# Performance work log

Hardware: AMD Instinct MI355X
Metric: run time of the kernel (lower is better)

Reference implementation:

```python
import jax, jax.numpy as jnp
import numpy as np

NUM_HEADS = 12


def setup_inputs() -> dict:
    key = jax.random.key(0)
    k1, k2, k3 = jax.random.split(key, 3)
    B, S, D = 2, 2048, 768
    x = jax.random.normal(k1, (B, S, D), dtype=jnp.float32)
    # torch Linear init: normal(std=0.002) weights, zero bias; stored as [in, out]
    W_qkv = jax.random.normal(k2, (D, 3 * D), dtype=jnp.float32) * 0.002
    b_qkv = jnp.zeros((3 * D,), dtype=jnp.float32)
    W_vw = jax.random.normal(k3, (D, D), dtype=jnp.float32) * 0.002
    b_vw = jnp.zeros((D,), dtype=jnp.float32)
    mask = jnp.ones((B, S), dtype=jnp.int32)  # padding mask, all valid
    return {"x": x, "W_qkv": W_qkv, "b_qkv": b_qkv, "W_vw": W_vw, "b_vw": b_vw, "mask": mask}


def reference(x, W_qkv, b_qkv, W_vw, b_vw, mask):
    B, S, D = x.shape
    H = NUM_HEADS
    Dh = D // H
    qkv = (x @ W_qkv + b_qkv).reshape(B, S, 3, H, Dh)
    q, k, v = qkv[:, :, 0], qkv[:, :, 1], qkv[:, :, 2]
    # [B, H, S, S] attention scores (full matrix, as in original)
    w = jnp.einsum('bshd,bzhd->bhsz', q, k)
    w = w / jnp.sqrt(jnp.asarray(Dh, dtype=x.dtype))  # scale=True
    # log-mask trick: padding mask [B,1,1,S] * causal tril [1,1,S,S]
    causal = jnp.tril(jnp.ones((S, S), dtype=x.dtype))
    wholemask = mask.astype(x.dtype)[:, None, None, :] * causal[None, None]
    w = w + jnp.log(wholemask)
    w = jax.nn.softmax(w, axis=-1)
    vw = jnp.einsum('bhsz,bzhd->bshd', w, v).reshape(B, S, D)
    return vw @ W_vw + b_vw
```

## Files before the change

kernel.cpp:

```cpp
#include <hip/hip_runtime.h>
#include <hip/hip_bf16.h>
#include <cmath>
#include <cstddef>

#define B_    2
#define S_    2048
#define D_    768
#define H_    12
#define DH_   64
#define NQKV_ 2304

typedef __attribute__((ext_vector_type(8))) short  short8;
typedef __attribute__((ext_vector_type(4))) float  floatx4;

__device__ __forceinline__ unsigned short f2bf(float f) {
    union { __hip_bfloat16 h; unsigned short u; } cv;
    cv.h = __float2bfloat16(f);
    return cv.u;
}

__device__ __forceinline__ void stage16(const unsigned short* g, unsigned short* ldsbase, int lane) {
#if __has_builtin(__builtin_amdgcn_global_load_lds)
    __builtin_amdgcn_global_load_lds(
        (const __attribute__((address_space(1))) unsigned int*)g,
        (__attribute__((address_space(3))) unsigned int*)ldsbase, 16, 0, 0);
#else
    *(short8*)(ldsbase + lane * 8) = *(const short8*)g;
#endif
}

__global__ void cvt_x_kernel(const float* __restrict__ x, unsigned short* __restrict__ xb)
{
    int i = (blockIdx.x * 256 + threadIdx.x) * 8;
    float4 a = *(const float4*)(x + i);
    float4 b = *(const float4*)(x + i + 4);
    short8 v;
    v[0] = (short)f2bf(a.x); v[1] = (short)f2bf(a.y);
    v[2] = (short)f2bf(a.z); v[3] = (short)f2bf(a.w);
    v[4] = (short)f2bf(b.x); v[5] = (short)f2bf(b.y);
    v[6] = (short)f2bf(b.z); v[7] = (short)f2bf(b.w);
    *(short8*)(xb + i) = v;
}

__global__ void cvt_w_kernel(const float* __restrict__ Wq, const float* __restrict__ Wv,
                             unsigned short* __restrict__ WqT, unsigned short* __restrict__ WvT)
{
    const int z = blockIdx.z;
    const int N = z ? D_ : NQKV_;
    if ((int)blockIdx.x * 32 >= N) return;
    const float* W = z ? Wv : Wq;
    unsigned short* WT = z ? WvT : WqT;

    __shared__ float t[32][33];
    const int tx = threadIdx.x, ty = threadIdx.y;
    const int n0 = blockIdx.x * 32, k0 = blockIdx.y * 32;
    #pragma unroll
    for (int i = 0; i < 4; ++i)
        t[ty + i * 8][tx] = W[(size_t)(k0 + ty + i * 8) * N + n0 + tx];
    __syncthreads();
    #pragma unroll
    for (int i = 0; i < 4; ++i)
        WT[(size_t)(n0 + ty + i * 8) * 768 + k0 + tx] = f2bf(t[tx][ty + i * 8]);
}

__global__ void vt_kernel(const unsigned short* __restrict__ V, unsigned short* __restrict__ VT)
{
    __shared__ unsigned short t[64][72];
    const int bh = blockIdx.x, s0 = blockIdx.y * 64;
    const unsigned short* src = V + ((size_t)bh * S_ + s0) * DH_;
    const int r = threadIdx.x >> 3, c = (threadIdx.x & 7) * 8;
    #pragma unroll
    for (int it = 0; it < 2; ++it)
        *(short8*)&t[r + it * 32][c] = *(const short8*)(src + (size_t)(r + it * 32) * DH_ + c);
    __syncthreads();
    #pragma unroll
    for (int it = 0; it < 2; ++it) {
        int d = r + it * 32;
        short8 v;
        #pragma unroll
        for (int i = 0; i < 8; ++i) v[i] = (short)t[c + i][d];
        *(short8*)(VT + ((size_t)bh * DH_ + d) * S_ + s0 + c) = v;
    }
}

__global__ __launch_bounds__(256, 2)
void mm_qkv_kernel(const unsigned short* __restrict__ A, const unsigned short* __restrict__ BT,
                   const float* __restrict__ bias,
                   unsigned short* __restrict__ Qo, unsigned short* __restrict__ Ko,
                   unsigned short* __restrict__ Vo)
{
    __shared__ unsigned short As[128][32];
    __shared__ unsigned short Bs[128][32];
    const int tid = threadIdx.x;
    const int wid = tid >> 6, lane = tid & 63;
    const int q = lane >> 4, ln = lane & 15;
    const int wm = (wid & 1) * 64, wn = (wid >> 1) * 64;
    const int m0 = blockIdx.y * 128, n0 = blockIdx.x * 128;
    const int lrow = wid * 16 + (lane >> 2);
    const int lcol = (lane & 3) * 8;
    const unsigned short* Ag = A  + (size_t)(m0 + lrow) * 768 + lcol;
    const unsigned short* Bg = BT + (size_t)(n0 + lrow) * 768 + lcol;

    floatx4 acc[4][4] = {};
    for (int k0 = 0; k0 < 768; k0 += 32) {
        __syncthreads();
        stage16(Ag + k0,            &As[wid * 16][0],      lane);
        stage16(Ag + k0 + 64 * 768, &As[64 + wid * 16][0], lane);
        stage16(Bg + k0,            &Bs[wid * 16][0],      lane);
        stage16(Bg + k0 + 64 * 768, &Bs[64 + wid * 16][0], lane);
        __syncthreads();
        short8 af[4], bf[4];
        #pragma unroll
        for (int mt = 0; mt < 4; ++mt) af[mt] = *(const short8*)&As[wm + mt * 16 + ln][q * 8];
        #pragma unroll
        for (int nt = 0; nt < 4; ++nt) bf[nt] = *(const short8*)&Bs[wn + nt * 16 + ln][q * 8];
        #pragma unroll
        for (int mt = 0; mt < 4; ++mt)
            #pragma unroll
            for (int nt = 0; nt < 4; ++nt)
                acc[mt][nt] = __builtin_amdgcn_mfma_f32_16x16x32_bf16(af[mt], bf[nt], acc[mt][nt], 0, 0, 0);
    }

    const int t = n0 / 768;
    unsigned short* __restrict__ dst = (t == 0) ? Qo : ((t == 1) ? Ko : Vo);
    const float qscale = (t == 0) ? 0.18033688011112042f : 1.0f;
    const int colb = n0 - t * 768 + wn;
    float bv[4];
    #pragma unroll
    for (int nt = 0; nt < 4; ++nt) bv[nt] = bias[n0 + wn + nt * 16 + ln];
    #pragma unroll
    for (int mt = 0; mt < 4; ++mt)
        #pragma unroll
        for (int r = 0; r < 4; ++r) {
            int row = m0 + wm + mt * 16 + q * 4 + r;
            int bb = row >> 11, s = row & 2047;
            #pragma unroll
            for (int nt = 0; nt < 4; ++nt) {
                int col = colb + nt * 16 + ln;
                int h = col >> 6, d = col & 63;
                dst[((size_t)(bb * H_ + h) * S_ + s) * DH_ + d] = f2bf((acc[mt][nt][r] + bv[nt]) * qscale);
            }
        }
}

__global__ __launch_bounds__(256, 2)
void flash8_kernel(const unsigned short* __restrict__ Qg, const unsigned short* __restrict__ Kg,
                   const unsigned short* __restrict__ VTg, const int* __restrict__ mask,
                   unsigned short* __restrict__ VW)
{
    __shared__ unsigned short Pl[4][32][40];
    __shared__ float Ol[32][68];
    __shared__ float li_s[4][32];

    const int tid = threadIdx.x;
    const int wid = tid >> 6, lane = tid & 63;
    const int q = lane >> 4, ln = lane & 15;
    const int bh = blockIdx.x % 24;
    const int pix = blockIdx.x / 24;
    const int b = bh / H_, h = bh % H_;

    const unsigned short* Qb = Qg  + (size_t)bh * S_ * DH_;
    const unsigned short* Kb = Kg  + (size_t)bh * S_ * DH_;
    const unsigned short* Vt = VTg + (size_t)bh * DH_ * S_;
    const int* mb = mask + b * S_;

    for (int half = 0; half < 2; ++half) {
        const int qt = half ? (63 - pix) : pix;
        const int r0 = qt * 32;
        const int T = qt + 1;

        short8 qf[2][2];
        #pragma unroll
        for (int mt = 0; mt < 2; ++mt)
            #pragma unroll
            for (int kk = 0; kk < 2; ++kk)
                qf[mt][kk] = *(const short8*)(Qb + (size_t)(r0 + mt * 16 + ln) * DH_ + kk * 32 + q * 8);

        floatx4 o[2][4] = {};
        float li[2][4] = {};

        for (int t = wid; t < T; t += 4) {
            const int z0 = t * 32;

            short8 kb[2][2];
            #pragma unroll
            for (int nt = 0; nt < 2; ++nt)
                #pragma unroll
                for (int kk = 0; kk < 2; ++kk)
                    kb[nt][kk] = *(const short8*)(Kb + (size_t)(z0 + nt * 16 + ln) * DH_ + kk * 32 + q * 8);

            short8 vb[4];
            #pragma unroll
            for (int dt = 0; dt < 4; ++dt)
                vb[dt] = *(const short8*)(Vt + (size_t)(dt * 16 + ln) * S_ + z0 + q * 8);

            const int m0i = mb[z0 + ln];
            const int m1i = mb[z0 + 16 + ln];

            floatx4 s[2][2] = {};
            __builtin_amdgcn_s_setprio(1);
            #pragma unroll
            for (int mt = 0; mt < 2; ++mt)
                #pragma unroll
                for (int nt = 0; nt < 2; ++nt) {
                    s[mt][nt] = __builtin_amdgcn_mfma_f32_16x16x32_bf16(qf[mt][0], kb[nt][0], s[mt][nt], 0, 0, 0);
                    s[mt][nt] = __builtin_amdgcn_mfma_f32_16x16x32_bf16(qf[mt][1], kb[nt][1], s[mt][nt], 0, 0, 0);
                }
            __builtin_amdgcn_s_setprio(0);

            const bool diag = (z0 + 31 > r0);
            if (__all(m0i && m1i) && !diag) {
                #pragma unroll
                for (int mt = 0; mt < 2; ++mt)
                    #pragma unroll
                    for (int nt = 0; nt < 2; ++nt)
                        #pragma unroll
                        for (int r = 0; r < 4; ++r) {
                            float p = exp2f(s[mt][nt][r]);
                            li[mt][r] += p;
                            Pl[wid][mt * 16 + q * 4 + r][nt * 16 + ln] = f2bf(p);
                        }
            } else {
                float mv[2];
                mv[0] = m0i ? 1.0f : 0.0f;
                mv[1] = m1i ? 1.0f : 0.0f;
                #pragma unroll
                for (int mt = 0; mt < 2; ++mt)
                    #pragma unroll
                    for (int nt = 0; nt < 2; ++nt) {
                        int z = z0 + nt * 16 + ln;
                        #pragma unroll
                        for (int r = 0; r < 4; ++r) {
                            float p = exp2f(s[mt][nt][r]) * mv[nt];
                            if (diag) {
                                int row = r0 + mt * 16 + q * 4 + r;
                                if (z > row) p = 0.0f;
                            }
                            li[mt][r] += p;
                            Pl[wid][mt * 16 + q * 4 + r][nt * 16 + ln] = f2bf(p);
                        }
                    }
            }

            #pragma unroll
            for (int mt = 0; mt < 2; ++mt) {
                short8 a = *(const short8*)&Pl[wid][mt * 16 + ln][q * 8];
                __builtin_amdgcn_s_setprio(1);
                #pragma unroll
                for (int dt = 0; dt < 4; ++dt)
                    o[mt][dt] = __builtin_amdgcn_mfma_f32_16x16x32_bf16(a, vb[dt], o[mt][dt], 0, 0, 0);
                __builtin_amdgcn_s_setprio(0);
            }
        }

        #pragma unroll
        for (int mt = 0; mt < 2; ++mt)
            #pragma unroll
            for (int r = 0; r < 4; ++r) {
                float v = li[mt][r];
                v += __shfl_xor(v, 1);
                v += __shfl_xor(v, 2);
                v += __shfl_xor(v, 4);
                v += __shfl_xor(v, 8);
                li[mt][r] = v;
            }

        #pragma unroll
        for (int w = 0; w < 4; ++w) {
            if (wid == w) {
                #pragma unroll
                for (int mt = 0; mt < 2; ++mt)
                    #pragma unroll
                    for (int r = 0; r < 4; ++r) {
                        int row = mt * 16 + q * 4 + r;
                        #pragma unroll
                        for (int dt = 0; dt < 4; ++dt) {
                            if (w == 0) Ol[row][dt * 16 + ln]  = o[mt][dt][r];
                            else        Ol[row][dt * 16 + ln] += o[mt][dt][r];
                        }
                        if (ln == 0) li_s[w][row] = li[mt][r];
                    }
            }
            __syncthreads();
        }

        {
            int row = tid >> 3, c = (tid & 7) * 8;
            float inv = 1.0f / (li_s[0][row] + li_s[1][row] + li_s[2][row] + li_s[3][row]);
            short8 ov;
            #pragma unroll
            for (int i = 0; i < 8; ++i) ov[i] = (short)f2bf(Ol[row][c + i] * inv);
            *(short8*)(VW + ((size_t)b * S_ + r0 + row) * D_ + h * DH_ + c) = ov;
        }
        __syncthreads();
    }
}

__global__ __launch_bounds__(256, 2)
void mm_proj_kernel(const unsigned short* __restrict__ A, const unsigned short* __restrict__ BT,
                    const float* __restrict__ bias, float* __restrict__ C)
{
    __shared__ unsigned short As[128][32];
    __shared__ unsigned short Bs[64][32];
    const int tid = threadIdx.x;
    const int wid = tid >> 6, lane = tid & 63;
    const int q = lane >> 4, ln = lane & 15;
    const int wm = (wid & 1) * 64, wn = (wid >> 1) * 32;
    const int m0 = blockIdx.y * 128, n0 = blockIdx.x * 64;
    const int lrow = wid * 16 + (lane >> 2);
    const int lcol = (lane & 3) * 8;
    const unsigned short* Ag = A  + (size_t)(m0 + lrow) * 768 + lcol;
    const unsigned short* Bg = BT + (size_t)(n0 + lrow) * 768 + lcol;

    floatx4 acc[4][2] = {};
    for (int k0 = 0; k0 < 768; k0 += 32) {
        __syncthreads();
        stage16(Ag + k0,            &As[wid * 16][0],      lane);
        stage16(Ag + k0 + 64 * 768, &As[64 + wid * 16][0], lane);
        stage16(Bg + k0,            &Bs[wid * 16][0],      lane);
        __syncthreads();
        short8 af[4], bf[2];
        #pragma unroll
        for (int mt = 0; mt < 4; ++mt) af[mt] = *(const short8*)&As[wm + mt * 16 + ln][q * 8];
        #pragma unroll
        for (int nt = 0; nt < 2; ++nt) bf[nt] = *(const short8*)&Bs[wn + nt * 16 + ln][q * 8];
        #pragma unroll
        for (int mt = 0; mt < 4; ++mt)
            #pragma unroll
            for (int nt = 0; nt < 2; ++nt)
                acc[mt][nt] = __builtin_amdgcn_mfma_f32_16x16x32_bf16(af[mt], bf[nt], acc[mt][nt], 0, 0, 0);
    }

    float bv[2];
    #pragma unroll
    for (int nt = 0; nt < 2; ++nt) bv[nt] = bias[n0 + wn + nt * 16 + ln];
    #pragma unroll
    for (int mt = 0; mt < 4; ++mt)
        #pragma unroll
        for (int r = 0; r < 4; ++r) {
            size_t row = (size_t)m0 + wm + mt * 16 + q * 4 + r;
            #pragma unroll
            for (int nt = 0; nt < 2; ++nt)
                C[row * D_ + n0 + wn + nt * 16 + ln] = acc[mt][nt][r] + bv[nt];
        }
}

extern "C" void kernel_launch(void* const* d_in, const int* in_sizes, int n_in,
                              void* d_out, int out_size, void* d_ws, size_t ws_size,
                              hipStream_t stream)
{
    (void)in_sizes; (void)n_in; (void)out_size; (void)ws_size;
    const float* x    = (const float*)d_in[0];
    const float* Wqkv = (const float*)d_in[1];
    const float* bqkv = (const float*)d_in[2];
    const float* Wvw  = (const float*)d_in[3];
    const float* bvw  = (const float*)d_in[4];
    const int*   mask = (const int*)d_in[5];
    float* out = (float*)d_out;

    const size_t XN  = (size_t)B_ * S_ * D_;
    unsigned short* ws  = (unsigned short*)d_ws;
    unsigned short* xb  = ws;
    unsigned short* WqT = xb  + XN;
    unsigned short* WvT = WqT + (size_t)NQKV_ * D_;
    unsigned short* Qb  = WvT + (size_t)D_ * D_;
    unsigned short* Kb  = Qb + XN;
    unsigned short* Vb  = Kb + XN;
    unsigned short* VbT = Vb + XN;
    unsigned short* VW  = VbT + XN;

    cvt_x_kernel<<<dim3(XN / (256 * 8)), 256, 0, stream>>>(x, xb);
    cvt_w_kernel<<<dim3(NQKV_ / 32, D_ / 32, 2), dim3(32, 8), 0, stream>>>(Wqkv, Wvw, WqT, WvT);
    mm_qkv_kernel<<<dim3(NQKV_ / 128, (B_ * S_) / 128), 256, 0, stream>>>(xb, WqT, bqkv, Qb, Kb, Vb);
    vt_kernel<<<dim3(B_ * H_, S_ / 64), 256, 0, stream>>>(Vb, VbT);
    flash8_kernel<<<dim3(24 * 32), 256, 0, stream>>>(Qb, Kb, VbT, mask, VW);
    mm_proj_kernel<<<dim3(D_ / 64, (B_ * S_) / 128), 256, 0, stream>>>(VW, WvT, bvw, out);
}
```

Before: 178.9 us.

## Compute transposed scores K·Qᵀ for packed P stores, one query tile per block

The attention kernel now computes the score tile as K times Q transposed, so each lane holds four consecutive key positions for one query row. This lets it write P to shared memory as packed 4-element vectors and reduce row sums over fewer shuffles. The kernel also drops the paired light/heavy query tiles per block and launches one block per query tile (twice the grid), ordered heaviest-first. In exchange it loses the built-in load balancing of the pairing and relies on the hardware scheduler to balance the uneven causal workloads.

```diff
diff --git a/kernel.cpp b/kernel.cpp
--- a/kernel.cpp
+++ b/kernel.cpp
@@ -11,6 +11,7 @@
 #define NQKV_ 2304
 
 typedef __attribute__((ext_vector_type(8))) short  short8;
+typedef __attribute__((ext_vector_type(4))) short  short4v;
 typedef __attribute__((ext_vector_type(4))) float  floatx4;
 
 __device__ __forceinline__ unsigned short f2bf(float f) {
@@ -144,7 +145,7 @@
 }
 
 __global__ __launch_bounds__(256, 2)
-void flash8_kernel(const unsigned short* __restrict__ Qg, const unsigned short* __restrict__ Kg,
+void flash9_kernel(const unsigned short* __restrict__ Qg, const unsigned short* __restrict__ Kg,
                    const unsigned short* __restrict__ VTg, const int* __restrict__ mask,
                    unsigned short* __restrict__ VW)
 {
@@ -156,143 +157,144 @@
     const int wid = tid >> 6, lane = tid & 63;
     const int q = lane >> 4, ln = lane & 15;
     const int bh = blockIdx.x % 24;
-    const int pix = blockIdx.x / 24;
+    const int qt = 63 - blockIdx.x / 24;
     const int b = bh / H_, h = bh % H_;
+    const int r0 = qt * 32;
 
     const unsigned short* Qb = Qg  + (size_t)bh * S_ * DH_;
     const unsigned short* Kb = Kg  + (size_t)bh * S_ * DH_;
     const unsigned short* Vt = VTg + (size_t)bh * DH_ * S_;
     const int* mb = mask + b * S_;
 
-    for (int half = 0; half < 2; ++half) {
-        const int qt = half ? (63 - pix) : pix;
-        const int r0 = qt * 32;
-        const int T = qt + 1;
-
-        short8 qf[2][2];
-        #pragma unroll
-        for (int mt = 0; mt < 2; ++mt)
+    short8 qf[2][2];
+    #pragma unroll
+    for (int rt = 0; rt < 2; ++rt)
+        #pragma unroll
+        for (int kk = 0; kk < 2; ++kk)
+            qf[rt][kk] = *(const short8*)(Qb + (size_t)(r0 + rt * 16 + ln) * DH_ + kk * 32 + q * 8);
+
+    floatx4 o[2][4] = {};
+    float li[2] = {};
+    const int T = qt + 1;
+
+    for (int t = wid; t < T; t += 4) {
+        const int z0 = t * 32;
+
+        short8 kf[2][2];
+        #pragma unroll
+        for (int zt = 0; zt < 2; ++zt)
             #pragma unroll
             for (int kk = 0; kk < 2; ++kk)
-                qf[mt][kk] = *(const short8*)(Qb + (size_t)(r0 + mt * 16 + ln) * DH_ + kk * 32 + q * 8);
-
-        floatx4 o[2][4] = {};
-        float li[2][4] = {};
-
-        for (int t = wid; t < T; t += 4) {
-            const int z0 = t * 32;
-
-            short8 kb[2][2];
-            #pragma unroll
-            for (int nt = 0; nt < 2; ++nt)
+                kf[zt][kk] = *(const short8*)(Kb + (size_t)(z0 + zt * 16 + ln) * DH_ + kk * 32 + q * 8);
+
+        short8 vb[4];
+        #pragma unroll
+        for (int dt = 0; dt < 4; ++dt)
+            vb[dt] = *(const short8*)(Vt + (size_t)(dt * 16 + ln) * S_ + z0 + q * 8);
+
+        const int mi = mb[z0 + (lane & 31)];
+
+        floatx4 s[2][2] = {};
+        __builtin_amdgcn_s_setprio(1);
+        #pragma unroll
+        for (int zt = 0; zt < 2; ++zt)
+            #pragma unroll
+            for (int rt = 0; rt < 2; ++rt) {
+                s[zt][rt] = __builtin_amdgcn_mfma_f32_16x16x32_bf16(kf[zt][0], qf[rt][0], s[zt][rt], 0, 0, 0);
+                s[zt][rt] = __builtin_amdgcn_mfma_f32_16x16x32_bf16(kf[zt][1], qf[rt][1], s[zt][rt], 0, 0, 0);
+            }
+        __builtin_amdgcn_s_setprio(0);
+
+        const bool diag = (z0 + 31 > r0);
+        if (__all(mi != 0) && !diag) {
+            #pragma unroll
+            for (int zt = 0; zt < 2; ++zt)
                 #pragma unroll
-                for (int kk = 0; kk < 2; ++kk)
-                    kb[nt][kk] = *(const short8*)(Kb + (size_t)(z0 + nt * 16 + ln) * DH_ + kk * 32 + q * 8);
-
-            short8 vb[4];
+                for (int rt = 0; rt < 2; ++rt) {
+                    float p0 = exp2f(s[zt][rt][0]);
+                    float p1 = exp2f(s[zt][rt][1]);
+                    float p2 = exp2f(s[zt][rt][2]);
+                    float p3 = exp2f(s[zt][rt][3]);
+                    li[rt] += (p0 + p1) + (p2 + p3);
+                    short4v pk;
+                    pk[0] = (short)f2bf(p0); pk[1] = (short)f2bf(p1);
+                    pk[2] = (short)f2bf(p2); pk[3] = (short)f2bf(p3);
+                    *(short4v*)&Pl[wid][rt * 16 + ln][zt * 16 + q * 4] = pk;
+                }
+        } else {
+            const int4 mA = *(const int4*)&mb[z0 + q * 4];
+            const int4 mB = *(const int4*)&mb[z0 + 16 + q * 4];
+            int ma[2][4];
+            ma[0][0] = mA.x; ma[0][1] = mA.y; ma[0][2] = mA.z; ma[0][3] = mA.w;
+            ma[1][0] = mB.x; ma[1][1] = mB.y; ma[1][2] = mB.z; ma[1][3] = mB.w;
+            #pragma unroll
+            for (int zt = 0; zt < 2; ++zt)
+                #pragma unroll
+                for (int rt = 0; rt < 2; ++rt) {
+                    const int zb = z0 + zt * 16 + q * 4;
+                    const int r  = r0 + rt * 16 + ln;
+                    float p[4];
+                    #pragma unroll
+                    for (int rr = 0; rr < 4; ++rr) {
+                        p[rr] = exp2f(s[zt][rt][rr]);
+                        if (!ma[zt][rr] || (zb + rr > r)) p[rr] = 0.0f;
+                    }
+                    li[rt] += (p[0] + p[1]) + (p[2] + p[3]);
+                    short4v pk;
+                    pk[0] = (short)f2bf(p[0]); pk[1] = (short)f2bf(p[1]);
+                    pk[2] = (short)f2bf(p[2]); pk[3] = (short)f2bf(p[3]);
+                    *(short4v*)&Pl[wid][rt * 16 + ln][zt * 16 + q * 4] = pk;
+                }
+        }
+
+        #pragma unroll
+        for (int mt = 0; mt < 2; ++mt) {
+            short8 a = *(const short8*)&Pl[wid][mt * 16 + ln][q * 8];
+            __builtin_amdgcn_s_setprio(1);
             #pragma unroll
             for (int dt = 0; dt < 4; ++dt)
-                vb[dt] = *(const short8*)(Vt + (size_t)(dt * 16 + ln) * S_ + z0 + q * 8);
-
-            const int m0i = mb[z0 + ln];
-            const int m1i = mb[z0 + 16 + ln];
-
-            floatx4 s[2][2] = {};
-            __builtin_amdgcn_s_setprio(1);
+                o[mt][dt] = __builtin_amdgcn_mfma_f32_16x16x32_bf16(a, vb[dt], o[mt][dt], 0, 0, 0);
+            __builtin_amdgcn_s_setprio(0);
+        }
+    }
+
+    #pragma unroll
+    for (int rt = 0; rt < 2; ++rt) {
+        float v = li[rt];
+        v += __shfl_xor(v, 16);
+        v += __shfl_xor(v, 32);
+        li[rt] = v;
+    }
+    if (lane < 16) {
+        li_s[wid][lane]      = li[0];
+        li_s[wid][16 + lane] = li[1];
+    }
+
+    #pragma unroll
+    for (int w = 0; w < 4; ++w) {
+        if (wid == w) {
             #pragma unroll
             for (int mt = 0; mt < 2; ++mt)
                 #pragma unroll
-                for (int nt = 0; nt < 2; ++nt) {
-                    s[mt][nt] = __builtin_amdgcn_mfma_f32_16x16x32_bf16(qf[mt][0], kb[nt][0], s[mt][nt], 0, 0, 0);
-                    s[mt][nt] = __builtin_amdgcn_mfma_f32_16x16x32_bf16(qf[mt][1], kb[nt][1], s[mt][nt], 0, 0, 0);
+                for (int r = 0; r < 4; ++r) {
+                    int row = mt * 16 + q * 4 + r;
+                    #pragma unroll
+                    for (int dt = 0; dt < 4; ++dt) {
+                        if (w == 0) Ol[row][dt * 16 + ln]  = o[mt][dt][r];
+                        else        Ol[row][dt * 16 + ln] += o[mt][dt][r];
+                    }
                 }
-            __builtin_amdgcn_s_setprio(0);
-
-            const bool diag = (z0 + 31 > r0);
-            if (__all(m0i && m1i) && !diag) {
-                #pragma unroll
-                for (int mt = 0; mt < 2; ++mt)
-                    #pragma unroll
-                    for (int nt = 0; nt < 2; ++nt)
-                        #pragma unroll
-                        for (int r = 0; r < 4; ++r) {
-                            float p = exp2f(s[mt][nt][r]);
-                            li[mt][r] += p;
-                            Pl[wid][mt * 16 + q * 4 + r][nt * 16 + ln] = f2bf(p);
-                        }
-            } else {
-                float mv[2];
-                mv[0] = m0i ? 1.0f : 0.0f;
-                mv[1] = m1i ? 1.0f : 0.0f;
-                #pragma unroll
-                for (int mt = 0; mt < 2; ++mt)
-                    #pragma unroll
-                    for (int nt = 0; nt < 2; ++nt) {
-                        int z = z0 + nt * 16 + ln;
-                        #pragma unroll
-                        for (int r = 0; r < 4; ++r) {
-                            float p = exp2f(s[mt][nt][r]) * mv[nt];
-                            if (diag) {
-                                int row = r0 + mt * 16 + q * 4 + r;
-                                if (z > row) p = 0.0f;
-                            }
-                            li[mt][r] += p;
-                            Pl[wid][mt * 16 + q * 4 + r][nt * 16 + ln] = f2bf(p);
-                        }
-                    }
-            }
-
-            #pragma unroll
-            for (int mt = 0; mt < 2; ++mt) {
-                short8 a = *(const short8*)&Pl[wid][mt * 16 + ln][q * 8];
-                __builtin_amdgcn_s_setprio(1);
-                #pragma unroll
-                for (int dt = 0; dt < 4; ++dt)
-                    o[mt][dt] = __builtin_amdgcn_mfma_f32_16x16x32_bf16(a, vb[dt], o[mt][dt], 0, 0, 0);
-                __builtin_amdgcn_s_setprio(0);
-            }
-        }
-
-        #pragma unroll
-        for (int mt = 0; mt < 2; ++mt)
-            #pragma unroll
-            for (int r = 0; r < 4; ++r) {
-                float v = li[mt][r];
-                v += __shfl_xor(v, 1);
-                v += __shfl_xor(v, 2);
-                v += __shfl_xor(v, 4);
-                v += __shfl_xor(v, 8);
-                li[mt][r] = v;
-            }
-
-        #pragma unroll
-        for (int w = 0; w < 4; ++w) {
-            if (wid == w) {
-                #pragma unroll
-                for (int mt = 0; mt < 2; ++mt)
-                    #pragma unroll
-                    for (int r = 0; r < 4; ++r) {
-                        int row = mt * 16 + q * 4 + r;
-                        #pragma unroll
-                        for (int dt = 0; dt < 4; ++dt) {
-                            if (w == 0) Ol[row][dt * 16 + ln]  = o[mt][dt][r];
-                            else        Ol[row][dt * 16 + ln] += o[mt][dt][r];
-                        }
-                        if (ln == 0) li_s[w][row] = li[mt][r];
-                    }
-            }
-            __syncthreads();
-        }
-
-        {
-            int row = tid >> 3, c = (tid & 7) * 8;
-            float inv = 1.0f / (li_s[0][row] + li_s[1][row] + li_s[2][row] + li_s[3][row]);
-            short8 ov;
-            #pragma unroll
-            for (int i = 0; i < 8; ++i) ov[i] = (short)f2bf(Ol[row][c + i] * inv);
-            *(short8*)(VW + ((size_t)b * S_ + r0 + row) * D_ + h * DH_ + c) = ov;
-        }
-        __syncthreads();
+        }
+        __syncthreads();
+    }
+
+    {
+        int row = tid >> 3, c = (tid & 7) * 8;
+        float inv = 1.0f / (li_s[0][row] + li_s[1][row] + li_s[2][row] + li_s[3][row]);
+        short8 ov;
+        #pragma unroll
+        for (int i = 0; i < 8; ++i) ov[i] = (short)f2bf(Ol[row][c + i] * inv);
+        *(short8*)(VW + ((size_t)b * S_ + r0 + row) * D_ + h * DH_ + c) = ov;
     }
 }
 
@@ -373,6 +375,6 @@
     cvt_w_kernel<<<dim3(NQKV_ / 32, D_ / 32, 2), dim3(32, 8), 0, stream>>>(Wqkv, Wvw, WqT, WvT);
     mm_qkv_kernel<<<dim3(NQKV_ / 128, (B_ * S_) / 128), 256, 0, stream>>>(xb, WqT, bqkv, Qb, Kb, Vb);
     vt_kernel<<<dim3(B_ * H_, S_ / 64), 256, 0, stream>>>(Vb, VbT);
-    flash8_kernel<<<dim3(24 * 32), 256, 0, stream>>>(Qb, Kb, VbT, mask, VW);
+    flash9_kernel<<<dim3(24 * 64), 256, 0, stream>>>(Qb, Kb, VbT, mask, VW);
     mm_proj_kernel<<<dim3(D_ / 64, (B_ * S_) / 128), 256, 0, stream>>>(VW, WvT, bvw, out);
 }
```

Result: no change. 179.9 us (+0.6%).
